# Kernel tuning notes

Hardware: AMD Instinct MI355X
Metric: run time of the kernel (lower is better)

Reference implementation:

```python
import jax, jax.numpy as jnp
import numpy as np
from jax import lax

B, TIN, N, TOUT, C = 8, 168, 1500, 24, 16
EMB, ALPHA, BETA, TOPK, DEPTH = 16, 1.5, 0.2, 12, 2
KERNELS = (2, 3, 6, 7)


def setup_inputs() -> dict:
    key = jax.random.key(0)
    ks = jax.random.split(key, 32)
    def rn(k, shape, scale=0.1):
        return jax.random.normal(k, shape, jnp.float32) * scale
    inp = {"x": jax.random.normal(ks[0], (B, TIN, N, 1), jnp.float32)}
    inp["pw"], inp["pb"] = rn(ks[1], (C, 1)), rn(ks[2], (C,))
    branch = C // len(KERNELS)
    for i, k in enumerate(KERNELS):
        inp[f"tw{k}"] = rn(ks[3 + 2 * i], (branch, C, 1, k))
        inp[f"tb{k}"] = rn(ks[4 + 2 * i], (branch,))
    inp["e1"], inp["e2"] = rn(ks[11], (N, EMB), 1.0), rn(ks[12], (N, EMB), 1.0)
    inp["gw1"], inp["gb1"] = rn(ks[13], (EMB, EMB)), rn(ks[14], (EMB,))
    inp["gw2"], inp["gb2"] = rn(ks[15], (EMB, EMB)), rn(ks[16], (EMB,))
    inp["mw"], inp["mb"] = rn(ks[17], (C, (DEPTH + 1) * C)), rn(ks[18], (C,))
    inp["rw1"], inp["rb1"] = rn(ks[19], (C, C)), rn(ks[20], (C,))
    inp["rw2"], inp["rb2"] = rn(ks[21], (TOUT, C)), rn(ks[22], (TOUT,))
    return inp


def _conv1x1(h, w, b):
    # h: [B, Cin, N, T], w: [Cout, Cin], b: [Cout]
    return jnp.einsum('bint,oi->bont', h, w) + b[None, :, None, None]


def _forward(x, pw, pb, tw2, tb2, tw3, tb3, tw6, tb6, tw7, tb7,
             e1, e2, gw1, gb1, gw2, gb2, mw, mb, rw1, rb1, rw2, rb2):
    h = jnp.transpose(x, (0, 3, 2, 1))                      # [B,1,N,TIN]
    h = _conv1x1(h, pw, pb)                                 # [B,C,N,TIN]
    # dilated inception: branches with kernels (2,3,6,7), truncate to shortest
    tlen = TIN - max(KERNELS) + 1
    outs = []
    for w, b in ((tw2, tb2), (tw3, tb3), (tw6, tb6), (tw7, tb7)):
        o = lax.conv_general_dilated(h, w, (1, 1), 'VALID',
                                     dimension_numbers=('NCHW', 'OIHW', 'NCHW'))
        outs.append(o[..., -tlen:] + b[None, :, None, None])
    h = jax.nn.relu(jnp.concatenate(outs, axis=1))          # [B,C,N,tlen]
    # adaptive top-k graph learning
    m1 = jnp.tanh(ALPHA * (e1 @ gw1 + gb1))
    m2 = jnp.tanh(ALPHA * (e2 @ gw2 + gb2))
    a = jax.nn.relu(jnp.tanh(ALPHA * (m1 @ m2.T - m2 @ m1.T)))  # [N,N]
    _, idx = lax.top_k(a, TOPK)
    mask = jnp.zeros((N, N), jnp.float32).at[jnp.arange(N)[:, None], idx].set(1.0)
    adj = a * mask
    # mix-hop graph convolution with row-normalized (A + I)
    adj = adj + jnp.eye(N, dtype=jnp.float32)
    adj = adj / jnp.sum(adj, axis=1, keepdims=True)
    hin = h
    hops = [h]
    for _ in range(DEPTH):
        h = BETA * hin + (1.0 - BETA) * jnp.einsum('bcwt,vw->bcvt', h, adj)
        hops.append(h)
    ho = jnp.concatenate(hops, axis=1)                      # [B,(D+1)C,N,tlen]
    h = jax.nn.relu(_conv1x1(ho, mw, mb))                   # [B,C,N,tlen]
    # dropout -> identity at inference
    r = jax.nn.relu(_conv1x1(h, rw1, rb1))
    y = _conv1x1(r, rw2, rb2)                               # [B,TOUT,N,tlen]
    return jnp.mean(y, axis=-1)                             # [B,TOUT,N]


def reference(x, pw, pb, tw2, tb2, tw3, tb3, tw6, tb6, tw7, tb7,
              e1, e2, gw1, gb1, gw2, gb2, mw, mb, rw1, rb1, rw2, rb2):
    return _forward(x, pw, pb, tw2, tb2, tw3, tb3, tw6, tb6, tw7, tb7,
                    e1, e2, gw1, gb1, gw2, gb2, mw, mb, rw1, rb1, rw2, rb2)
```

## Files before the change

### kernel.cpp

```cpp
#include <hip/hip_runtime.h>

#define BB 8
#define TIN 168
#define NN 1500
#define TOUTC 24
#define TLEN 162
#define NG 32
#define NTH 768
#define SN 2
#define TOPKK 12
#define NTILE 94
#define NPAD 1504

#define OFF_M1   0
#define OFF_M2   24000
#define OFF_M1T  48000
#define OFF_M2T  72000
#define OFF_EW   96000
#define OFF_EB   96112
#define OFF_ADJW 96128
#define OFF_ADJI 115628
#define OFF_FR   135128
#define OFF_S16  136664
#define OFF_PART 328664

typedef __attribute__((ext_vector_type(8))) short short8;
typedef __attribute__((ext_vector_type(4))) float v4f;

__device__ __forceinline__ unsigned short f2bf(float f) {
    unsigned int u = __float_as_uint(f);
    unsigned int r = (u + 0x7fffu + ((u >> 16) & 1u)) >> 16;
    return (unsigned short)r;
}
__device__ __forceinline__ unsigned int pack2(float lo, float hi) {
    return (unsigned int)f2bf(lo) | ((unsigned int)f2bf(hi) << 16);
}
__device__ __forceinline__ float unlo(unsigned int u) { return __uint_as_float(u << 16); }
__device__ __forceinline__ float unhi(unsigned int u) { return __uint_as_float(u & 0xffff0000u); }
__device__ __forceinline__ float bf2f(unsigned short s) { return __uint_as_float(((unsigned int)s) << 16); }

__device__ __forceinline__ short8 as_s8(uint4 u) { union { uint4 a; short8 b; } c; c.a = u; return c.b; }

__global__ __launch_bounds__(256) void prep_kernel(
    const float* __restrict__ e1, const float* __restrict__ e2,
    const float* __restrict__ gw1, const float* __restrict__ gb1,
    const float* __restrict__ gw2, const float* __restrict__ gb2,
    const float* __restrict__ pw, const float* __restrict__ pb,
    const float* __restrict__ tw2, const float* __restrict__ tb2,
    const float* __restrict__ tw3, const float* __restrict__ tb3,
    const float* __restrict__ tw6, const float* __restrict__ tb6,
    const float* __restrict__ tw7, const float* __restrict__ tb7,
    const float* __restrict__ mw, const float* __restrict__ rw1,
    float* __restrict__ ws)
{
    int n = blockIdx.x * blockDim.x + threadIdx.x;
    if (n < NN) {
        float a1[16], a2[16];
        #pragma unroll
        for (int o = 0; o < 16; ++o) { a1[o] = gb1[o]; a2[o] = gb2[o]; }
        #pragma unroll
        for (int i = 0; i < 16; ++i) {
            float u = e1[n*16+i], v = e2[n*16+i];
            #pragma unroll
            for (int o = 0; o < 16; ++o) {
                a1[o] += u * gw1[i*16+o];
                a2[o] += v * gw2[i*16+o];
            }
        }
        #pragma unroll
        for (int o = 0; o < 16; ++o) {
            float t1v = tanhf(1.5f*a1[o]);
            float t2v = tanhf(1.5f*a2[o]);
            ws[OFF_M1 + n*16+o] = t1v;
            ws[OFF_M2 + n*16+o] = t2v;
            ws[OFF_M1T + o*NN + n] = t1v;
            ws[OFF_M2T + o*NN + n] = t2v;
        }
    }
    if (blockIdx.x == 0 && threadIdx.x < 16) {
        int c = threadIdx.x;
        int br = c >> 2, oc = c & 3;
        const float* tw; const float* tb; int k;
        if (br == 0)      { tw = tw2; tb = tb2; k = 2; }
        else if (br == 1) { tw = tw3; tb = tb3; k = 3; }
        else if (br == 2) { tw = tw6; tb = tb6; k = 6; }
        else              { tw = tw7; tb = tb7; k = 7; }
        for (int d = 0; d < 7; ++d) ws[OFF_EW + c*7 + d] = 0.f;
        float ebv = tb[oc];
        for (int j = 0; j < k; ++j) {
            float s = 0.f, sb = 0.f;
            for (int ic = 0; ic < 16; ++ic) {
                float w = tw[(oc*16+ic)*k + j];
                s  += w * pw[ic];
                sb += w * pb[ic];
            }
            ws[OFF_EW + c*7 + (7-k+j)] = s;
            ebv += sb;
        }
        ws[OFF_EB + c] = ebv;
    }
    if (blockIdx.x == 1 && threadIdx.x < 64) {
        int lane = threadIdx.x;
        int m = lane & 15, q = lane >> 4;
        unsigned short* frw = (unsigned short*)(ws + OFF_FR);
        for (int mat = 0; mat < 3; ++mat) {
            for (int j = 0; j < 8; ++j) {
                int k = q*8 + j;
                float s;
                if (mat == 0) s = (k < 16) ? mw[m*48+k] + 0.2f*(mw[m*48+16+k] + mw[m*48+32+k])
                                           : 0.8f*mw[m*48+16+(k-16)] + 0.16f*mw[m*48+32+(k-16)];
                else if (mat == 1) s = (k < 16) ? 0.64f*mw[m*48+32+k] : 0.f;
                else               s = (k < 16) ? rw1[m*16+k] : 0.f;
                unsigned short hi = f2bf(s);
                unsigned short lo = f2bf(s - bf2f(hi));
                frw[(mat*2+0)*512 + lane*8 + j] = hi;
                frw[(mat*2+1)*512 + lane*8 + j] = lo;
            }
        }
    }
}

__global__ __launch_bounds__(256) void graph_kernel(
    const float* __restrict__ m1, const float* __restrict__ m2,
    const float* __restrict__ m1T, const float* __restrict__ m2T,
    float* __restrict__ adjw, int* __restrict__ adji)
{
    int v = blockIdx.x;
    int tid = threadIdx.x;
    __shared__ float wv4[4];
    __shared__ int   wi4[4];
    __shared__ int   bcast_i;
    __shared__ float m1v[16], m2v[16];
    if (tid < 16) { m1v[tid] = m1[v*16+tid]; m2v[tid] = m2[v*16+tid]; }
    __syncthreads();
    float sreg[6];
    #pragma unroll
    for (int u = 0; u < 6; ++u) {
        int j = tid + 256*u;
        float a = -1.f;
        if (j < NN) {
            float d = 0.f;
            #pragma unroll
            for (int i = 0; i < 16; ++i)
                d += m1v[i]*m2T[i*NN+j] - m2v[i]*m1T[i*NN+j];
            float t = tanhf(1.5f*d);
            a = t > 0.f ? t : 0.f;
        }
        sreg[u] = a;
    }
    float lb = -1.f; int li = NN;
    #pragma unroll
    for (int u = 0; u < 6; ++u) {
        int j = tid + 256*u;
        if (j < NN && sreg[u] > lb) { lb = sreg[u]; li = j; }
    }
    const int wid = tid >> 6;
    for (int it = 0; it < TOPKK; ++it) {
        float bv = lb; int bi = li;
        #pragma unroll
        for (int off = 32; off > 0; off >>= 1) {
            float ov = __shfl_down(bv, off);
            int   oi = __shfl_down(bi, off);
            if (ov > bv || (ov == bv && oi < bi)) { bv = ov; bi = oi; }
        }
        if ((tid & 63) == 0) { wv4[wid] = bv; wi4[wid] = bi; }
        __syncthreads();
        if (tid == 0) {
            #pragma unroll
            for (int w = 1; w < 4; ++w) {
                float ov = wv4[w]; int oi = wi4[w];
                if (ov > bv || (ov == bv && oi < bi)) { bv = ov; bi = oi; }
            }
            adjw[v*13+it] = bv;
            adji[v*13+it] = bi;
            bcast_i = bi;
        }
        __syncthreads();
        int win = bcast_i;
        if (li == win) {
            #pragma unroll
            for (int u = 0; u < 6; ++u)
                if (tid + 256*u == win) sreg[u] = -1.f;
            lb = -1.f; li = NN;
            #pragma unroll
            for (int u = 0; u < 6; ++u) {
                int j = tid + 256*u;
                if (j < NN && sreg[u] > lb) { lb = sreg[u]; li = j; }
            }
        }
    }
    if (tid == 0) {
        float s = 1.f;
        #pragma unroll
        for (int it = 0; it < TOPKK; ++it) s += adjw[v*13+it];
        float inv = 1.f/s;
        #pragma unroll
        for (int it = 0; it < TOPKK; ++it) adjw[v*13+it] *= inv;
        adji[v*13+12] = v;
        adjw[v*13+12] = inv;
    }
}

__device__ __forceinline__ short8 ldfrag(const unsigned short* fr, int plane, int lane) {
    const uint4* p = (const uint4*)(fr + plane*512);
    return as_s8(p[lane]);
}

__global__ __launch_bounds__(NTH, 3) void main_kernel(
    const float* __restrict__ x,
    const float* __restrict__ ew, const float* __restrict__ eb,
    const float* __restrict__ adjw, const int* __restrict__ adji,
    const unsigned short* __restrict__ fr,
    float* __restrict__ part,
    const float* __restrict__ mb, const float* __restrict__ rb1)
{
    __shared__ uint4 feat[6][NPAD];

    const int tid = threadIdx.x;
    const int lane = tid & 63;
    const int wid = tid >> 6;
    const int b = blockIdx.x >> 5;
    const int g = blockIdx.x & 31;
    const int t0 = (g*TLEN) >> 5;
    const int t1 = ((g+1)*TLEN) >> 5;
    const int n0 = lane & 15, q = lane >> 4;
    float* partBG = part + (size_t)(b*NG + g)*NN*16;

    #pragma unroll 1
    for (int s = 0; s < SN; ++s) {
        int v = tid + NTH*s;
        if (v < NN) {
            float xv[7];
            #pragma unroll
            for (int d = 0; d < 7; ++d) xv[d] = x[(b*TIN + t0 + d)*NN + v];
            float h[16];
            #pragma unroll
            for (int c = 0; c < 16; ++c) {
                float a = eb[c];
                #pragma unroll
                for (int d = 0; d < 7; ++d) a += ew[c*7+d]*xv[d];
                h[c] = a > 0.f ? a : 0.f;
            }
            feat[0][v] = make_uint4(pack2(h[0],h[1]), pack2(h[2],h[3]), pack2(h[4],h[5]), pack2(h[6],h[7]));
            feat[1][v] = make_uint4(pack2(h[8],h[9]), pack2(h[10],h[11]), pack2(h[12],h[13]), pack2(h[14],h[15]));
        }
    }
    __syncthreads();

    for (int t = t0; t < t1; ++t) {
        const int par = (t - t0) & 1;
        const int hc = par ? 4 : 0;
        const int hn = par ? 0 : 4;

        #pragma unroll 1
        for (int s = 0; s < SN; ++s) {
            int v = tid + NTH*s;
            if (v < NN) {
                float u1[16];
                #pragma unroll
                for (int c = 0; c < 16; ++c) u1[c] = 0.f;
                int base = v*13;
                #pragma unroll
                for (int j = 0; j < 13; ++j) {
                    int nb = adji[base+j];
                    float w = adjw[base+j];
                    uint4 b0 = feat[hc][nb], b1 = feat[hc+1][nb];
                    unsigned int uu[8] = {b0.x,b0.y,b0.z,b0.w,b1.x,b1.y,b1.z,b1.w};
                    #pragma unroll
                    for (int i = 0; i < 8; ++i) { u1[2*i] += w*unlo(uu[i]); u1[2*i+1] += w*unhi(uu[i]); }
                }
                feat[2][v] = make_uint4(pack2(u1[0],u1[1]), pack2(u1[2],u1[3]), pack2(u1[4],u1[5]), pack2(u1[6],u1[7]));
                feat[3][v] = make_uint4(pack2(u1[8],u1[9]), pack2(u1[10],u1[11]), pack2(u1[12],u1[13]), pack2(u1[14],u1[15]));
            }
        }
        __syncthreads();

        {
            short8 a1h = ldfrag(fr, 0, lane), a1l = ldfrag(fr, 1, lane);
            short8 a2h = ldfrag(fr, 2, lane), a2l = ldfrag(fr, 3, lane);
            ushort4* zH = (ushort4*)feat[hc + (q >> 1)];
            ushort4* pH = (ushort4*)feat[2  + (q >> 1)];
            #pragma unroll 1
            for (int T = wid; T < NTILE; T += 12) {
                int n = T*16 + n0;
                short8 bf  = as_s8(feat[(q < 2) ? (hc + q) : q][n]);
                short8 b2f = as_s8(feat[2 + (q & 1)][n]);
                v4f z = {0.f,0.f,0.f,0.f}, p = {0.f,0.f,0.f,0.f};
                z = __builtin_amdgcn_mfma_f32_16x16x32_bf16(a1h, bf, z, 0, 0, 0);
                z = __builtin_amdgcn_mfma_f32_16x16x32_bf16(a1l, bf, z, 0, 0, 0);
                p = __builtin_amdgcn_mfma_f32_16x16x32_bf16(a2h, b2f, p, 0, 0, 0);
                p = __builtin_amdgcn_mfma_f32_16x16x32_bf16(a2l, b2f, p, 0, 0, 0);
                ushort4 zz; zz.x = f2bf(z[0]); zz.y = f2bf(z[1]); zz.z = f2bf(z[2]); zz.w = f2bf(z[3]);
                ushort4 pp; pp.x = f2bf(p[0]); pp.y = f2bf(p[1]); pp.z = f2bf(p[2]); pp.w = f2bf(p[3]);
                zH[n*2 + (q & 1)] = zz;
                pH[n*2 + (q & 1)] = pp;
            }
        }
        __syncthreads();

        if (t + 1 < t1) {
            #pragma unroll 1
            for (int s = 0; s < SN; ++s) {
                int v = tid + NTH*s;
                if (v < NN) {
                    float xv[7];
                    #pragma unroll
                    for (int d = 0; d < 7; ++d) xv[d] = x[(b*TIN + (t+1) + d)*NN + v];
                    float h[16];
                    #pragma unroll
                    for (int c = 0; c < 16; ++c) {
                        float a = eb[c];
                        #pragma unroll
                        for (int d = 0; d < 7; ++d) a += ew[c*7+d]*xv[d];
                        h[c] = a > 0.f ? a : 0.f;
                    }
                    feat[hn][v]   = make_uint4(pack2(h[0],h[1]), pack2(h[2],h[3]), pack2(h[4],h[5]), pack2(h[6],h[7]));
                    feat[hn+1][v] = make_uint4(pack2(h[8],h[9]), pack2(h[10],h[11]), pack2(h[12],h[13]), pack2(h[14],h[15]));
                }
            }
        }
        {
            short8 a3h = ldfrag(fr, 4, lane), a3l = ldfrag(fr, 5, lane);
            float mbq[4], rbq[4];
            #pragma unroll
            for (int r = 0; r < 4; ++r) { mbq[r] = mb[q*4+r]; rbq[r] = rb1[q*4+r]; }
            ushort4* zH = (ushort4*)feat[hc + (q >> 1)];
            const ushort4* pH = (const ushort4*)feat[2 + (q >> 1)];
            #pragma unroll 1
            for (int T = wid; T < NTILE; T += 12) {
                int n = T*16 + n0;
                ushort4 zz = zH[n*2 + (q & 1)];
                float y0 = mbq[0] + bf2f(zz.x);
                float y1 = mbq[1] + bf2f(zz.y);
                float y2 = mbq[2] + bf2f(zz.z);
                float y3 = mbq[3] + bf2f(zz.w);
                int base = (n < NN ? n : NN-1) * 13;
                #pragma unroll
                for (int j = 0; j < 13; ++j) {
                    int nb = adji[base+j];
                    float w = adjw[base+j];
                    ushort4 ps = pH[nb*2 + (q & 1)];
                    y0 += w*bf2f(ps.x); y1 += w*bf2f(ps.y);
                    y2 += w*bf2f(ps.z); y3 += w*bf2f(ps.w);
                }
                y0 = y0 > 0.f ? y0 : 0.f;  y1 = y1 > 0.f ? y1 : 0.f;
                y2 = y2 > 0.f ? y2 : 0.f;  y3 = y3 > 0.f ? y3 : 0.f;
                ushort4 yy; yy.x = f2bf(y0); yy.y = f2bf(y1); yy.z = f2bf(y2); yy.w = f2bf(y3);
                zH[n*2 + (q & 1)] = yy;
                short8 bfY = as_s8(feat[(q < 2) ? (hc + q) : q][n]);
                v4f acc = {0.f,0.f,0.f,0.f};
                acc = __builtin_amdgcn_mfma_f32_16x16x32_bf16(a3h, bfY, acc, 0, 0, 0);
                acc = __builtin_amdgcn_mfma_f32_16x16x32_bf16(a3l, bfY, acc, 0, 0, 0);
                if (n < NN) {
                    float r0 = acc[0]+rbq[0], r1 = acc[1]+rbq[1], r2 = acc[2]+rbq[2], r3 = acc[3]+rbq[3];
                    r0 = r0 > 0.f ? r0 : 0.f;  r1 = r1 > 0.f ? r1 : 0.f;
                    r2 = r2 > 0.f ? r2 : 0.f;  r3 = r3 > 0.f ? r3 : 0.f;
                    float4* pp = (float4*)(partBG + (size_t)n*16 + q*4);
                    if (t == t0) {
                        *pp = make_float4(r0, r1, r2, r3);
                    } else {
                        float4 o = *pp;
                        *pp = make_float4(o.x+r0, o.y+r1, o.z+r2, o.w+r3);
                    }
                }
            }
        }
        __syncthreads();
    }
}

__global__ __launch_bounds__(256) void reduce1_kernel(const float* __restrict__ part,
                                                      float* __restrict__ s16buf)
{
    int idx = blockIdx.x*256 + threadIdx.x;
    if (idx >= BB*NN*16) return;
    int c = idx & 15;
    int rest = idx >> 4;
    int v = rest % NN;
    int b = rest / NN;
    float s = 0.f;
    #pragma unroll
    for (int g = 0; g < NG; ++g)
        s += part[((size_t)(b*NG + g)*NN + v)*16 + c];
    s16buf[idx] = s * (1.0f/TLEN);
}

__global__ __launch_bounds__(256) void reduce2_kernel(const float* __restrict__ s16buf,
                                                      const float* __restrict__ rw2,
                                                      const float* __restrict__ rb2,
                                                      float* __restrict__ out)
{
    int idx = blockIdx.x*256 + threadIdx.x;
    if (idx >= BB*NN) return;
    int v = idx % NN;
    int b = idx / NN;
    const float4* sp = (const float4*)(s16buf + (size_t)idx*16);
    float4 s0 = sp[0], s1 = sp[1], s2 = sp[2], s3 = sp[3];
    float s16[16] = {s0.x,s0.y,s0.z,s0.w, s1.x,s1.y,s1.z,s1.w,
                     s2.x,s2.y,s2.z,s2.w, s3.x,s3.y,s3.z,s3.w};
    #pragma unroll
    for (int o = 0; o < TOUTC; ++o) {
        float a = rb2[o];
        #pragma unroll
        for (int c = 0; c < 16; ++c) a += rw2[o*16+c]*s16[c];
        out[(b*TOUTC + o)*NN + v] = a;
    }
}

extern "C" void kernel_launch(void* const* d_in, const int* in_sizes, int n_in,
                              void* d_out, int out_size, void* d_ws, size_t ws_size,
                              hipStream_t stream)
{
    const float* x   = (const float*)d_in[0];
    const float* pw  = (const float*)d_in[1];
    const float* pb  = (const float*)d_in[2];
    const float* tw2 = (const float*)d_in[3];
    const float* tb2 = (const float*)d_in[4];
    const float* tw3 = (const float*)d_in[5];
    const float* tb3 = (const float*)d_in[6];
    const float* tw6 = (const float*)d_in[7];
    const float* tb6 = (const float*)d_in[8];
    const float* tw7 = (const float*)d_in[9];
    const float* tb7 = (const float*)d_in[10];
    const float* e1  = (const float*)d_in[11];
    const float* e2  = (const float*)d_in[12];
    const float* gw1 = (const float*)d_in[13];
    const float* gb1 = (const float*)d_in[14];
    const float* gw2 = (const float*)d_in[15];
    const float* gb2 = (const float*)d_in[16];
    const float* mw  = (const float*)d_in[17];
    const float* mb  = (const float*)d_in[18];
    const float* rw1 = (const float*)d_in[19];
    const float* rb1 = (const float*)d_in[20];
    const float* rw2 = (const float*)d_in[21];
    const float* rb2 = (const float*)d_in[22];
    float* ws  = (float*)d_ws;
    float* out = (float*)d_out;

    prep_kernel<<<(NN + 255)/256, 256, 0, stream>>>(e1,e2,gw1,gb1,gw2,gb2,pw,pb,
                                                    tw2,tb2,tw3,tb3,tw6,tb6,tw7,tb7,
                                                    mw, rw1, ws);
    graph_kernel<<<NN, 256, 0, stream>>>(ws + OFF_M1, ws + OFF_M2,
                                         ws + OFF_M1T, ws + OFF_M2T,
                                         ws + OFF_ADJW, (int*)ws + OFF_ADJI);
    main_kernel<<<BB*NG, NTH, 0, stream>>>(x, ws + OFF_EW, ws + OFF_EB,
                                           ws + OFF_ADJW, (const int*)ws + OFF_ADJI,
                                           (const unsigned short*)(ws + OFF_FR),
                                           ws + OFF_PART, mb, rb1);
    reduce1_kernel<<<(BB*NN*16 + 255)/256, 256, 0, stream>>>(ws + OFF_PART, ws + OFF_S16);
    reduce2_kernel<<<(BB*NN + 255)/256, 256, 0, stream>>>(ws + OFF_S16, rw2, rb2, out);
}
```

Before: 297.2 us.

## Switch packed features to fp16, interleave adjacency, keep z tiles in registers

Replaces software bf16 rounding with hardware packed fp16 conversion (cvt_pkrtz) and moves the MFMAs to the f16 variant. The adjacency weights and indices are interleaved into one float2 array laid out column-major, so neighbour loads are coalesced. The z tiles from the first MFMA phase stay in registers across the barrier instead of being written to and read back from shared memory. The tile loops are fully unrolled. These changes cut ALU work for conversions and shared-memory traffic, at the cost of higher register pressure and fp16 range limits on the activations.

```diff
diff --git a/kernel.cpp b/kernel.cpp
--- a/kernel.cpp
+++ b/kernel.cpp
@@ -18,28 +18,25 @@
 #define OFF_M2T  72000
 #define OFF_EW   96000
 #define OFF_EB   96112
-#define OFF_ADJW 96128
-#define OFF_ADJI 115628
+#define OFF_ADJ  96128
 #define OFF_FR   135128
 #define OFF_S16  136664
 #define OFF_PART 328664
 
-typedef __attribute__((ext_vector_type(8))) short short8;
+typedef __attribute__((ext_vector_type(8))) _Float16 half8;
+typedef __attribute__((ext_vector_type(2))) _Float16 half2v;
 typedef __attribute__((ext_vector_type(4))) float v4f;
 
-__device__ __forceinline__ unsigned short f2bf(float f) {
-    unsigned int u = __float_as_uint(f);
-    unsigned int r = (u + 0x7fffu + ((u >> 16) & 1u)) >> 16;
-    return (unsigned short)r;
-}
-__device__ __forceinline__ unsigned int pack2(float lo, float hi) {
-    return (unsigned int)f2bf(lo) | ((unsigned int)f2bf(hi) << 16);
-}
-__device__ __forceinline__ float unlo(unsigned int u) { return __uint_as_float(u << 16); }
-__device__ __forceinline__ float unhi(unsigned int u) { return __uint_as_float(u & 0xffff0000u); }
-__device__ __forceinline__ float bf2f(unsigned short s) { return __uint_as_float(((unsigned int)s) << 16); }
-
-__device__ __forceinline__ short8 as_s8(uint4 u) { union { uint4 a; short8 b; } c; c.a = u; return c.b; }
+__device__ __forceinline__ unsigned int pk2(float lo, float hi) {
+    return __builtin_bit_cast(unsigned int, __builtin_amdgcn_cvt_pkrtz(lo, hi));
+}
+__device__ __forceinline__ float h2lo(unsigned int u) {
+    return (float)__builtin_bit_cast(half2v, u).x;
+}
+__device__ __forceinline__ float h2hi(unsigned int u) {
+    return (float)__builtin_bit_cast(half2v, u).y;
+}
+__device__ __forceinline__ half8 as_h8(uint4 u) { return __builtin_bit_cast(half8, u); }
 
 __global__ __launch_bounds__(256) void prep_kernel(
     const float* __restrict__ e1, const float* __restrict__ e2,
@@ -101,20 +98,20 @@
     }
     if (blockIdx.x == 1 && threadIdx.x < 64) {
         int lane = threadIdx.x;
-        int m = lane & 15, q = lane >> 4;
+        int m = lane & 15, qq = lane >> 4;
         unsigned short* frw = (unsigned short*)(ws + OFF_FR);
         for (int mat = 0; mat < 3; ++mat) {
             for (int j = 0; j < 8; ++j) {
-                int k = q*8 + j;
+                int k = qq*8 + j;
                 float s;
                 if (mat == 0) s = (k < 16) ? mw[m*48+k] + 0.2f*(mw[m*48+16+k] + mw[m*48+32+k])
                                            : 0.8f*mw[m*48+16+(k-16)] + 0.16f*mw[m*48+32+(k-16)];
                 else if (mat == 1) s = (k < 16) ? 0.64f*mw[m*48+32+k] : 0.f;
                 else               s = (k < 16) ? rw1[m*16+k] : 0.f;
-                unsigned short hi = f2bf(s);
-                unsigned short lo = f2bf(s - bf2f(hi));
-                frw[(mat*2+0)*512 + lane*8 + j] = hi;
-                frw[(mat*2+1)*512 + lane*8 + j] = lo;
+                _Float16 hi = (_Float16)s;
+                _Float16 lo = (_Float16)(s - (float)hi);
+                frw[(mat*2+0)*512 + lane*8 + j] = __builtin_bit_cast(unsigned short, hi);
+                frw[(mat*2+1)*512 + lane*8 + j] = __builtin_bit_cast(unsigned short, lo);
             }
         }
     }
@@ -123,7 +120,7 @@
 __global__ __launch_bounds__(256) void graph_kernel(
     const float* __restrict__ m1, const float* __restrict__ m2,
     const float* __restrict__ m1T, const float* __restrict__ m2T,
-    float* __restrict__ adjw, int* __restrict__ adji)
+    float2* __restrict__ adj)
 {
     int v = blockIdx.x;
     int tid = threadIdx.x;
@@ -155,6 +152,8 @@
         if (j < NN && sreg[u] > lb) { lb = sreg[u]; li = j; }
     }
     const int wid = tid >> 6;
+    float kw[TOPKK]; int ki[TOPKK];
+    #pragma unroll
     for (int it = 0; it < TOPKK; ++it) {
         float bv = lb; int bi = li;
         #pragma unroll
@@ -171,8 +170,7 @@
                 float ov = wv4[w]; int oi = wi4[w];
                 if (ov > bv || (ov == bv && oi < bi)) { bv = ov; bi = oi; }
             }
-            adjw[v*13+it] = bv;
-            adji[v*13+it] = bi;
+            kw[it] = bv; ki[it] = bi;
             bcast_i = bi;
         }
         __syncthreads();
@@ -192,24 +190,24 @@
     if (tid == 0) {
         float s = 1.f;
         #pragma unroll
-        for (int it = 0; it < TOPKK; ++it) s += adjw[v*13+it];
+        for (int it = 0; it < TOPKK; ++it) s += kw[it];
         float inv = 1.f/s;
         #pragma unroll
-        for (int it = 0; it < TOPKK; ++it) adjw[v*13+it] *= inv;
-        adji[v*13+12] = v;
-        adjw[v*13+12] = inv;
-    }
-}
-
-__device__ __forceinline__ short8 ldfrag(const unsigned short* fr, int plane, int lane) {
+        for (int it = 0; it < TOPKK; ++it)
+            adj[it*NN + v] = make_float2(kw[it]*inv, __int_as_float(ki[it]));
+        adj[TOPKK*NN + v] = make_float2(inv, __int_as_float(v));
+    }
+}
+
+__device__ __forceinline__ half8 ldfrag(const unsigned short* fr, int plane, int lane) {
     const uint4* p = (const uint4*)(fr + plane*512);
-    return as_s8(p[lane]);
+    return as_h8(p[lane]);
 }
 
 __global__ __launch_bounds__(NTH, 3) void main_kernel(
     const float* __restrict__ x,
     const float* __restrict__ ew, const float* __restrict__ eb,
-    const float* __restrict__ adjw, const int* __restrict__ adji,
+    const float2* __restrict__ adj,
     const unsigned short* __restrict__ fr,
     float* __restrict__ part,
     const float* __restrict__ mb, const float* __restrict__ rb1)
@@ -241,8 +239,8 @@
                 for (int d = 0; d < 7; ++d) a += ew[c*7+d]*xv[d];
                 h[c] = a > 0.f ? a : 0.f;
             }
-            feat[0][v] = make_uint4(pack2(h[0],h[1]), pack2(h[2],h[3]), pack2(h[4],h[5]), pack2(h[6],h[7]));
-            feat[1][v] = make_uint4(pack2(h[8],h[9]), pack2(h[10],h[11]), pack2(h[12],h[13]), pack2(h[14],h[15]));
+            feat[0][v] = make_uint4(pk2(h[0],h[1]), pk2(h[2],h[3]), pk2(h[4],h[5]), pk2(h[6],h[7]));
+            feat[1][v] = make_uint4(pk2(h[8],h[9]), pk2(h[10],h[11]), pk2(h[12],h[13]), pk2(h[14],h[15]));
         }
     }
     __syncthreads();
@@ -259,41 +257,43 @@
                 float u1[16];
                 #pragma unroll
                 for (int c = 0; c < 16; ++c) u1[c] = 0.f;
-                int base = v*13;
                 #pragma unroll
                 for (int j = 0; j < 13; ++j) {
-                    int nb = adji[base+j];
-                    float w = adjw[base+j];
+                    float2 aw = adj[j*NN + v];
+                    float w = aw.x;
+                    int nb = __float_as_int(aw.y);
                     uint4 b0 = feat[hc][nb], b1 = feat[hc+1][nb];
                     unsigned int uu[8] = {b0.x,b0.y,b0.z,b0.w,b1.x,b1.y,b1.z,b1.w};
                     #pragma unroll
-                    for (int i = 0; i < 8; ++i) { u1[2*i] += w*unlo(uu[i]); u1[2*i+1] += w*unhi(uu[i]); }
+                    for (int i = 0; i < 8; ++i) { u1[2*i] += w*h2lo(uu[i]); u1[2*i+1] += w*h2hi(uu[i]); }
                 }
-                feat[2][v] = make_uint4(pack2(u1[0],u1[1]), pack2(u1[2],u1[3]), pack2(u1[4],u1[5]), pack2(u1[6],u1[7]));
-                feat[3][v] = make_uint4(pack2(u1[8],u1[9]), pack2(u1[10],u1[11]), pack2(u1[12],u1[13]), pack2(u1[14],u1[15]));
+                feat[2][v] = make_uint4(pk2(u1[0],u1[1]), pk2(u1[2],u1[3]), pk2(u1[4],u1[5]), pk2(u1[6],u1[7]));
+                feat[3][v] = make_uint4(pk2(u1[8],u1[9]), pk2(u1[10],u1[11]), pk2(u1[12],u1[13]), pk2(u1[14],u1[15]));
             }
         }
         __syncthreads();
 
+        v4f zsv[8];
         {
-            short8 a1h = ldfrag(fr, 0, lane), a1l = ldfrag(fr, 1, lane);
-            short8 a2h = ldfrag(fr, 2, lane), a2l = ldfrag(fr, 3, lane);
-            ushort4* zH = (ushort4*)feat[hc + (q >> 1)];
-            ushort4* pH = (ushort4*)feat[2  + (q >> 1)];
-            #pragma unroll 1
-            for (int T = wid; T < NTILE; T += 12) {
-                int n = T*16 + n0;
-                short8 bf  = as_s8(feat[(q < 2) ? (hc + q) : q][n]);
-                short8 b2f = as_s8(feat[2 + (q & 1)][n]);
-                v4f z = {0.f,0.f,0.f,0.f}, p = {0.f,0.f,0.f,0.f};
-                z = __builtin_amdgcn_mfma_f32_16x16x32_bf16(a1h, bf, z, 0, 0, 0);
-                z = __builtin_amdgcn_mfma_f32_16x16x32_bf16(a1l, bf, z, 0, 0, 0);
-                p = __builtin_amdgcn_mfma_f32_16x16x32_bf16(a2h, b2f, p, 0, 0, 0);
-                p = __builtin_amdgcn_mfma_f32_16x16x32_bf16(a2l, b2f, p, 0, 0, 0);
-                ushort4 zz; zz.x = f2bf(z[0]); zz.y = f2bf(z[1]); zz.z = f2bf(z[2]); zz.w = f2bf(z[3]);
-                ushort4 pp; pp.x = f2bf(p[0]); pp.y = f2bf(p[1]); pp.z = f2bf(p[2]); pp.w = f2bf(p[3]);
-                zH[n*2 + (q & 1)] = zz;
-                pH[n*2 + (q & 1)] = pp;
+            half8 a1h = ldfrag(fr, 0, lane), a1l = ldfrag(fr, 1, lane);
+            half8 a2h = ldfrag(fr, 2, lane), a2l = ldfrag(fr, 3, lane);
+            uint2* pH = (uint2*)feat[2 + (q >> 1)];
+            #pragma unroll
+            for (int it = 0; it < 8; ++it) {
+                int T = wid + 12*it;
+                if (T < NTILE) {
+                    int n = T*16 + n0;
+                    half8 bf  = as_h8(feat[(q < 2) ? (hc + q) : q][n]);
+                    half8 b2f = as_h8(feat[2 + (q & 1)][n]);
+                    v4f z = {0.f,0.f,0.f,0.f}, p = {0.f,0.f,0.f,0.f};
+                    z = __builtin_amdgcn_mfma_f32_16x16x32_f16(a1h, bf, z, 0, 0, 0);
+                    z = __builtin_amdgcn_mfma_f32_16x16x32_f16(a1l, bf, z, 0, 0, 0);
+                    p = __builtin_amdgcn_mfma_f32_16x16x32_f16(a2h, b2f, p, 0, 0, 0);
+                    p = __builtin_amdgcn_mfma_f32_16x16x32_f16(a2l, b2f, p, 0, 0, 0);
+                    zsv[it] = z;
+                    uint2 ppk; ppk.x = pk2(p[0], p[1]); ppk.y = pk2(p[2], p[3]);
+                    pH[n*2 + (q & 1)] = ppk;
+                }
             }
         }
         __syncthreads();
@@ -314,53 +314,57 @@
                         for (int d = 0; d < 7; ++d) a += ew[c*7+d]*xv[d];
                         h[c] = a > 0.f ? a : 0.f;
                     }
-                    feat[hn][v]   = make_uint4(pack2(h[0],h[1]), pack2(h[2],h[3]), pack2(h[4],h[5]), pack2(h[6],h[7]));
-                    feat[hn+1][v] = make_uint4(pack2(h[8],h[9]), pack2(h[10],h[11]), pack2(h[12],h[13]), pack2(h[14],h[15]));
+                    feat[hn][v]   = make_uint4(pk2(h[0],h[1]), pk2(h[2],h[3]), pk2(h[4],h[5]), pk2(h[6],h[7]));
+                    feat[hn+1][v] = make_uint4(pk2(h[8],h[9]), pk2(h[10],h[11]), pk2(h[12],h[13]), pk2(h[14],h[15]));
                 }
             }
         }
         {
-            short8 a3h = ldfrag(fr, 4, lane), a3l = ldfrag(fr, 5, lane);
+            half8 a3h = ldfrag(fr, 4, lane), a3l = ldfrag(fr, 5, lane);
             float mbq[4], rbq[4];
             #pragma unroll
             for (int r = 0; r < 4; ++r) { mbq[r] = mb[q*4+r]; rbq[r] = rb1[q*4+r]; }
-            ushort4* zH = (ushort4*)feat[hc + (q >> 1)];
-            const ushort4* pH = (const ushort4*)feat[2 + (q >> 1)];
-            #pragma unroll 1
-            for (int T = wid; T < NTILE; T += 12) {
-                int n = T*16 + n0;
-                ushort4 zz = zH[n*2 + (q & 1)];
-                float y0 = mbq[0] + bf2f(zz.x);
-                float y1 = mbq[1] + bf2f(zz.y);
-                float y2 = mbq[2] + bf2f(zz.z);
-                float y3 = mbq[3] + bf2f(zz.w);
-                int base = (n < NN ? n : NN-1) * 13;
-                #pragma unroll
-                for (int j = 0; j < 13; ++j) {
-                    int nb = adji[base+j];
-                    float w = adjw[base+j];
-                    ushort4 ps = pH[nb*2 + (q & 1)];
-                    y0 += w*bf2f(ps.x); y1 += w*bf2f(ps.y);
-                    y2 += w*bf2f(ps.z); y3 += w*bf2f(ps.w);
-                }
-                y0 = y0 > 0.f ? y0 : 0.f;  y1 = y1 > 0.f ? y1 : 0.f;
-                y2 = y2 > 0.f ? y2 : 0.f;  y3 = y3 > 0.f ? y3 : 0.f;
-                ushort4 yy; yy.x = f2bf(y0); yy.y = f2bf(y1); yy.z = f2bf(y2); yy.w = f2bf(y3);
-                zH[n*2 + (q & 1)] = yy;
-                short8 bfY = as_s8(feat[(q < 2) ? (hc + q) : q][n]);
-                v4f acc = {0.f,0.f,0.f,0.f};
-                acc = __builtin_amdgcn_mfma_f32_16x16x32_bf16(a3h, bfY, acc, 0, 0, 0);
-                acc = __builtin_amdgcn_mfma_f32_16x16x32_bf16(a3l, bfY, acc, 0, 0, 0);
-                if (n < NN) {
-                    float r0 = acc[0]+rbq[0], r1 = acc[1]+rbq[1], r2 = acc[2]+rbq[2], r3 = acc[3]+rbq[3];
-                    r0 = r0 > 0.f ? r0 : 0.f;  r1 = r1 > 0.f ? r1 : 0.f;
-                    r2 = r2 > 0.f ? r2 : 0.f;  r3 = r3 > 0.f ? r3 : 0.f;
-                    float4* pp = (float4*)(partBG + (size_t)n*16 + q*4);
-                    if (t == t0) {
-                        *pp = make_float4(r0, r1, r2, r3);
-                    } else {
-                        float4 o = *pp;
-                        *pp = make_float4(o.x+r0, o.y+r1, o.z+r2, o.w+r3);
+            uint2* zH = (uint2*)feat[hc + (q >> 1)];
+            const uint2* pH = (const uint2*)feat[2 + (q >> 1)];
+            #pragma unroll
+            for (int it = 0; it < 8; ++it) {
+                int T = wid + 12*it;
+                if (T < NTILE) {
+                    int n = T*16 + n0;
+                    float y0 = mbq[0] + zsv[it][0];
+                    float y1 = mbq[1] + zsv[it][1];
+                    float y2 = mbq[2] + zsv[it][2];
+                    float y3 = mbq[3] + zsv[it][3];
+                    int vc = n < NN ? n : NN-1;
+                    #pragma unroll
+                    for (int j = 0; j < 13; ++j) {
+                        float2 aw = adj[j*NN + vc];
+                        float w = aw.x;
+                        int nb = __float_as_int(aw.y);
+                        uint2 ps = pH[nb*2 + (q & 1)];
+                        y0 += w*h2lo(ps.x); y1 += w*h2hi(ps.x);
+                        y2 += w*h2lo(ps.y); y3 += w*h2hi(ps.y);
+                    }
+                    y0 = y0 > 0.f ? y0 : 0.f;  y1 = y1 > 0.f ? y1 : 0.f;
+                    y2 = y2 > 0.f ? y2 : 0.f;  y3 = y3 > 0.f ? y3 : 0.f;
+                    uint2 ypk; ypk.x = pk2(y0, y1); ypk.y = pk2(y2, y3);
+                    zH[n*2 + (q & 1)] = ypk;
+                    asm volatile("" ::: "memory");
+                    half8 bfY = as_h8(feat[(q < 2) ? (hc + q) : q][n]);
+                    v4f acc = {0.f,0.f,0.f,0.f};
+                    acc = __builtin_amdgcn_mfma_f32_16x16x32_f16(a3h, bfY, acc, 0, 0, 0);
+                    acc = __builtin_amdgcn_mfma_f32_16x16x32_f16(a3l, bfY, acc, 0, 0, 0);
+                    if (n < NN) {
+                        float r0 = acc[0]+rbq[0], r1 = acc[1]+rbq[1], r2 = acc[2]+rbq[2], r3 = acc[3]+rbq[3];
+                        r0 = r0 > 0.f ? r0 : 0.f;  r1 = r1 > 0.f ? r1 : 0.f;
+                        r2 = r2 > 0.f ? r2 : 0.f;  r3 = r3 > 0.f ? r3 : 0.f;
+                        float4* pp = (float4*)(partBG + (size_t)n*16 + q*4);
+                        if (t == t0) {
+                            *pp = make_float4(r0, r1, r2, r3);
+                        } else {
+                            float4 o = *pp;
+                            *pp = make_float4(o.x+r0, o.y+r1, o.z+r2, o.w+r3);
+                        }
                     }
                 }
             }
@@ -442,9 +446,9 @@
                                                     mw, rw1, ws);
     graph_kernel<<<NN, 256, 0, stream>>>(ws + OFF_M1, ws + OFF_M2,
                                          ws + OFF_M1T, ws + OFF_M2T,
-                                         ws + OFF_ADJW, (int*)ws + OFF_ADJI);
+                                         (float2*)(ws + OFF_ADJ));
     main_kernel<<<BB*NG, NTH, 0, stream>>>(x, ws + OFF_EW, ws + OFF_EB,
-                                           ws + OFF_ADJW, (const int*)ws + OFF_ADJI,
+                                           (const float2*)(ws + OFF_ADJ),
                                            (const unsigned short*)(ws + OFF_FR),
                                            ws + OFF_PART, mb, rb1);
     reduce1_kernel<<<(BB*NN*16 + 255)/256, 256, 0, stream>>>(ws + OFF_PART, ws + OFF_S16);
```

Result: slower. 619.8 us (+108.6%).
